# Kernel optimization log

Hardware: AMD Instinct MI355X
Metric: run time of the kernel (lower is better)

The kernel has to match this reference:

```python
import jax, jax.numpy as jnp
import numpy as np

EPS = 1e-5


def _ligru_layer(x, W, U, gamma, beta):
    """One bidirectional LiGRU layer. x: (B,T,F) -> (B,T,2H)."""
    B = x.shape[0]
    H = U.shape[1]
    # bidirectional: stack forward copy and time-flipped copy along batch
    x2 = jnp.concatenate([x, x[:, ::-1]], axis=0)  # (2B, T, F)
    w = jnp.einsum('btf,gf->btg', x2, W)           # (2B, T, 2H)
    # training-mode BatchNorm1d over flattened (2B*T, 2H), biased variance
    flat = w.reshape(-1, w.shape[-1])
    mean = flat.mean(axis=0)
    var = flat.var(axis=0)
    w = (w - mean) * jax.lax.rsqrt(var + EPS) * gamma + beta

    def step(h, wt):
        gates = wt + h @ U.T            # (2B, 2H)
        at, zt = gates[:, :H], gates[:, H:]
        z = jax.nn.sigmoid(zt)
        h = z * h + (1.0 - z) * jax.nn.relu(at)
        return h, h

    h0 = jnp.zeros((w.shape[0], H), dtype=w.dtype)
    _, hs = jax.lax.scan(step, h0, jnp.swapaxes(w, 0, 1))  # (T, 2B, H)
    hs = jnp.swapaxes(hs, 0, 1)                            # (2B, T, H)
    h_f, h_b = hs[:B], hs[B:, ::-1]                        # un-flip backward dir
    return jnp.concatenate([h_f, h_b], axis=2)             # (B, T, 2H)


def setup_inputs() -> dict:
    key = jax.random.key(0)
    ks = jax.random.split(key, 9)
    B, T, F, H = 16, 500, 512, 1024
    return {
        'x': jax.random.normal(ks[0], (B, T, F), jnp.float32),
        'w0': jax.random.normal(ks[1], (2 * H, F), jnp.float32) * (1.0 / np.sqrt(F)),
        'u0': jax.random.normal(ks[2], (2 * H, H), jnp.float32) * (1.0 / np.sqrt(H)),
        'g0': jax.random.uniform(ks[3], (2 * H,), jnp.float32, 0.5, 1.5),
        'b0': jax.random.normal(ks[4], (2 * H,), jnp.float32) * 0.1,
        'w1': jax.random.normal(ks[5], (2 * H, 2 * H), jnp.float32) * (1.0 / np.sqrt(2 * H)),
        'u1': jax.random.normal(ks[6], (2 * H, H), jnp.float32) * (1.0 / np.sqrt(H)),
        'g1': jax.random.uniform(ks[7], (2 * H,), jnp.float32, 0.5, 1.5),
        'b1': jax.random.normal(ks[8], (2 * H,), jnp.float32) * 0.1,
    }


def reference(x, w0, u0, g0, b0, w1, u1, g1, b1):
    h = _ligru_layer(x, w0, u0, g0, b0)   # (B, T, 2H)
    h = _ligru_layer(h, w1, u1, g1, b1)   # (B, T, 2H)
    return h
```

## Files before the change

kernel.cpp:

```cpp
#include <hip/hip_runtime.h>
#include <stdint.h>

#define KT 500
#define KH 1024
#define KG 2048

typedef short bf16x8 __attribute__((ext_vector_type(8)));
typedef float f32x4 __attribute__((ext_vector_type(4)));

__device__ __forceinline__ unsigned short f2bf(float f){
  union { float f; unsigned int i; } u; u.f = f;
  unsigned int x = u.i;
  return (unsigned short)((x + 0x7fffu + ((x >> 16) & 1u)) >> 16);
}
__device__ __forceinline__ float bf2f(unsigned short h){
  union { unsigned int i; float f; } u; u.i = ((unsigned int)h) << 16;
  return u.f;
}

__device__ __forceinline__ void load_b128_dev(uint4& dst, const void* p){
  asm volatile("global_load_dwordx4 %0, %1, off sc1"
               : "=v"(dst) : "v"(p) : "memory");
}
__device__ __forceinline__ void store_b32_dev(void* p, unsigned int v){
  asm volatile("global_store_dword %0, %1, off sc1"
               :: "v"(p), "v"(v) : "memory");
}
__device__ __forceinline__ void wait_vm0(){
  asm volatile("s_waitcnt vmcnt(0)" ::: "memory");
}

__global__ __launch_bounds__(256) void castk(const float* __restrict__ s,
                                             unsigned short* __restrict__ d, int n4){
  int i = blockIdx.x*256 + threadIdx.x;
  if (i >= n4) return;
  float4 v = ((const float4*)s)[i];
  unsigned int lo = (unsigned int)f2bf(v.x) | ((unsigned int)f2bf(v.y) << 16);
  unsigned int hi = (unsigned int)f2bf(v.z) | ((unsigned int)f2bf(v.w) << 16);
  ((uint2*)d)[i] = make_uint2(lo, hi);
}

template<int MODE, int KDIM>
__global__ __launch_bounds__(256) void gemm_bn(
    const unsigned short* __restrict__ A,
    const unsigned short* __restrict__ Bw,
    unsigned short* __restrict__ Wout)
{
  __shared__ __attribute__((aligned(16))) unsigned short As[128*72];
  __shared__ __attribute__((aligned(16))) unsigned short Bs[128*72];
  const int tid = threadIdx.x;
  const int lane = tid & 63, wid = tid >> 6;
  const int ntile = blockIdx.x, mtile = blockIdx.y;
  const int arow_loc = tid >> 3;
  const int k8 = tid & 7;

  long abaseLo[4], abaseHi[4], bbase[4];
  #pragma unroll
  for (int i = 0; i < 4; i++){
    int r = mtile*128 + i*32 + arow_loc;
    int s = r / KT;
    int t = r - s*KT;
    if (MODE == 0){
      abaseLo[i] = (s < 16) ? (long)((s*KT + t)*512)
                            : (long)(((s-16)*KT + (KT-1-t))*512);
      abaseHi[i] = 0;
    } else {
      int sp = s & 15;
      int rev = (s >= 16);
      abaseLo[i] = (long)((sp*KT + (rev ? KT-1-t : t)) * KH);
      abaseHi[i] = (long)(((16+sp)*KT + (rev ? t : KT-1-t)) * KH);
    }
    bbase[i] = (long)(ntile*128 + i*32 + arow_loc) * KDIM;
  }

  f32x4 acc[4][4];
  #pragma unroll
  for (int a=0;a<4;a++)
    #pragma unroll
    for (int b=0;b<4;b++)
      acc[a][b] = (f32x4){0.f,0.f,0.f,0.f};

  const int mhalf = wid & 1, nhalf = wid >> 1;
  const int lrow = lane & 15, quad = lane >> 4;

  for (int k0 = 0; k0 < KDIM; k0 += 64){
    const int kel = k0 + k8*8;
    #pragma unroll
    for (int i = 0; i < 4; i++){
      long aoff;
      if (MODE == 0) aoff = abaseLo[i] + kel;
      else           aoff = (kel < KH) ? (abaseLo[i] + kel) : (abaseHi[i] + (kel - KH));
      uint4 va = *(const uint4*)(A + aoff);
      uint4 vb = *(const uint4*)(Bw + bbase[i] + kel);
      *(uint4*)&As[(i*32 + arow_loc)*72 + k8*8] = va;
      *(uint4*)&Bs[(i*32 + arow_loc)*72 + k8*8] = vb;
    }
    __syncthreads();
    #pragma unroll
    for (int kk = 0; kk < 64; kk += 32){
      bf16x8 af[4], bfr[4];
      #pragma unroll
      for (int mt=0; mt<4; mt++)
        af[mt] = *(const bf16x8*)&As[(mhalf*64 + mt*16 + lrow)*72 + kk + quad*8];
      #pragma unroll
      for (int nt=0; nt<4; nt++)
        bfr[nt] = *(const bf16x8*)&Bs[(nhalf*64 + nt*16 + lrow)*72 + kk + quad*8];
      #pragma unroll
      for (int mt=0; mt<4; mt++)
        #pragma unroll
        for (int nt=0; nt<4; nt++)
          acc[mt][nt] = __builtin_amdgcn_mfma_f32_16x16x32_bf16(af[mt], bfr[nt], acc[mt][nt], 0, 0, 0);
    }
    __syncthreads();
  }

  #pragma unroll
  for (int mt=0; mt<4; mt++)
    #pragma unroll
    for (int nt=0; nt<4; nt++)
      #pragma unroll
      for (int r=0; r<4; r++){
        int grow = mtile*128 + mhalf*64 + mt*16 + quad*4 + r;
        int gcol = ntile*128 + nhalf*64 + nt*16 + lrow;
        Wout[(long)grow*KG + gcol] = f2bf(acc[mt][nt][r]);
      }
}

__global__ __launch_bounds__(256) void bn_partial(const unsigned short* __restrict__ W,
                                                  float* __restrict__ part){
  const int blk = blockIdx.x, tid = threadIdx.x;
  const int c0 = tid*8;
  float s[8], qq[8];
  #pragma unroll
  for (int j=0;j<8;j++){ s[j]=0.f; qq[j]=0.f; }
  const unsigned short* base = W + (long)blk*128*KG + c0;
  for (int r=0;r<128;r++){
    uint4 v = *(const uint4*)(base + (long)r*KG);
    unsigned int w[4] = {v.x, v.y, v.z, v.w};
    #pragma unroll
    for (int p=0;p<4;p++){
      union { unsigned int i; float f; } lo, hi;
      lo.i = w[p] << 16;
      hi.i = w[p] & 0xffff0000u;
      s[2*p]   += lo.f; qq[2*p]   += lo.f*lo.f;
      s[2*p+1] += hi.f; qq[2*p+1] += hi.f*hi.f;
    }
  }
  float* pd = part + (long)blk*4096;
  #pragma unroll
  for (int j=0;j<8;j++){ pd[c0+j] = s[j]; pd[KG + c0 + j] = qq[j]; }
}

__global__ __launch_bounds__(256) void bn_final(const float* __restrict__ part,
                                                const float* __restrict__ gamma,
                                                const float* __restrict__ beta,
                                                float* __restrict__ scsh){
  int g = blockIdx.x*256 + threadIdx.x;
  float s=0.f, qq=0.f;
  for (int b=0;b<125;b++){ s += part[(long)b*4096 + g]; qq += part[(long)b*4096 + KG + g]; }
  float mean = s * (1.f/16000.f);
  float var  = qq * (1.f/16000.f) - mean*mean;
  float sc = gamma[g] * rsqrtf(var + 1e-5f);
  scsh[g]      = sc;
  scsh[KG + g] = beta[g] - mean*sc;
}

template<int LAYER>
__global__ __launch_bounds__(256, 1) void recur(
    const unsigned short* __restrict__ Ub,
    const unsigned short* __restrict__ Wn,
    const float* __restrict__ scsh,
    unsigned short* __restrict__ hbuf,
    int* __restrict__ flags,
    unsigned short* __restrict__ hsOut,
    float* __restrict__ out)
{
  __shared__ __attribute__((aligned(16))) unsigned short Ush[32*1032];
  __shared__ __attribute__((aligned(16))) unsigned short hsh[32*1032];
  __shared__ float gA[32*20];
  __shared__ float gZ[32*20];
  __shared__ float hown[512];
  __shared__ float scA[16], shA[16], scZ[16], shZ[16];

  const int tid = threadIdx.x;
  const int q = blockIdx.x;
  const int ga = q*16;

  #pragma unroll
  for (int i=0;i<16;i++){
    int c = i*256 + tid;
    int row = c >> 7, k8c = c & 127;
    int grow = (row < 16) ? (ga + row) : (KH + ga + row - 16);
    uint4 v = *(const uint4*)(Ub + (long)grow*KH + k8c*8);
    *(uint4*)&Ush[row*1032 + k8c*8] = v;
  }
  if (tid < 64){
    int j = tid & 15, w = tid >> 4;
    if      (w==0) scA[j] = scsh[ga+j];
    else if (w==1) shA[j] = scsh[KG + ga + j];
    else if (w==2) scZ[j] = scsh[KH + ga + j];
    else           shZ[j] = scsh[KG + KH + ga + j];
  }
  hown[tid] = 0.f; hown[tid+256] = 0.f;
  __syncthreads();

  const int lane = tid & 63, wid = tid >> 6;
  const int lrow = lane & 15, quad = lane >> 4;
  const int mhalf = wid & 1, ghalf = wid >> 1;
  const int es = tid >> 3, ep = tid & 7;
  const int r0 = tid >> 7, kc = tid & 127;

  for (int t = 0; t < KT; t++){
    const unsigned short* wr = Wn + (long)(es*KT + t)*KG + ga + 2*ep;
    unsigned int wa01 = *(const unsigned int*)(wr);
    unsigned int wz01 = *(const unsigned int*)(wr + KH);
    asm volatile("" ::: "memory");

    if (t > 0 && tid < 64){
      while (__hip_atomic_load(&flags[(t-1)*64 + tid], __ATOMIC_RELAXED,
                               __HIP_MEMORY_SCOPE_AGENT) == 0){}
    }
    __syncthreads();

    const unsigned short* hb = hbuf + (t & 1)*32768 + r0*KH + kc*8;
    uint4 hreg[16];
    #pragma unroll
    for (int i=0;i<16;i++)
      load_b128_dev(hreg[i], hb + i*2048);
    wait_vm0();
    #pragma unroll
    for (int i=0;i<16;i++)
      *(uint4*)&hsh[(2*i + r0)*1032 + kc*8] = hreg[i];
    __syncthreads();

    f32x4 a0 = (f32x4){0,0,0,0}, a1 = a0, a2 = a0, a3 = a0;
    const unsigned short* ar = &hsh[(mhalf*16 + lrow)*1032 + quad*8];
    const unsigned short* br = &Ush[(ghalf*16 + lrow)*1032 + quad*8];
    #pragma unroll
    for (int k0=0;k0<KH;k0+=128){
      a0 = __builtin_amdgcn_mfma_f32_16x16x32_bf16(*(const bf16x8*)(ar+k0),    *(const bf16x8*)(br+k0),    a0,0,0,0);
      a1 = __builtin_amdgcn_mfma_f32_16x16x32_bf16(*(const bf16x8*)(ar+k0+32), *(const bf16x8*)(br+k0+32), a1,0,0,0);
      a2 = __builtin_amdgcn_mfma_f32_16x16x32_bf16(*(const bf16x8*)(ar+k0+64), *(const bf16x8*)(br+k0+64), a2,0,0,0);
      a3 = __builtin_amdgcn_mfma_f32_16x16x32_bf16(*(const bf16x8*)(ar+k0+96), *(const bf16x8*)(br+k0+96), a3,0,0,0);
    }
    f32x4 accs = (a0 + a1) + (a2 + a3);
    float* gd = ghalf ? gZ : gA;
    #pragma unroll
    for (int r=0;r<4;r++)
      gd[(mhalf*16 + quad*4 + r)*20 + lrow] = accs[r];
    __syncthreads();

    float2 gav = *(const float2*)&gA[es*20 + 2*ep];
    float2 gzv = *(const float2*)&gZ[es*20 + 2*ep];
    float2 hpv = *(const float2*)&hown[es*16 + 2*ep];
    float2 scav = *(const float2*)&scA[2*ep];
    float2 shav = *(const float2*)&shA[2*ep];
    float2 sczv = *(const float2*)&scZ[2*ep];
    float2 shzv = *(const float2*)&shZ[2*ep];
    float aa0 = gav.x + bf2f((unsigned short)(wa01 & 0xffff)) * scav.x + shav.x;
    float aa1 = gav.y + bf2f((unsigned short)(wa01 >> 16))    * scav.y + shav.y;
    float zz0 = gzv.x + bf2f((unsigned short)(wz01 & 0xffff)) * sczv.x + shzv.x;
    float zz1 = gzv.y + bf2f((unsigned short)(wz01 >> 16))    * sczv.y + shzv.y;
    float z0 = 1.f/(1.f + __expf(-zz0));
    float z1 = 1.f/(1.f + __expf(-zz1));
    float hn0 = z0*hpv.x + (1.f - z0)*fmaxf(aa0, 0.f);
    float hn1 = z1*hpv.y + (1.f - z1)*fmaxf(aa1, 0.f);
    *(float2*)&hown[es*16 + 2*ep] = make_float2(hn0, hn1);

    unsigned int hpack = (unsigned int)f2bf(hn0) | ((unsigned int)f2bf(hn1) << 16);
    store_b32_dev(hbuf + ((t+1)&1)*32768 + es*KH + ga + 2*ep, hpack);
    wait_vm0();
    __syncthreads();
    if (tid == 0)
      __hip_atomic_store(&flags[t*64 + q], 1, __ATOMIC_RELAXED, __HIP_MEMORY_SCOPE_AGENT);

    if (LAYER == 0){
      *(unsigned int*)&hsOut[(long)(es*KT + t)*KH + ga + 2*ep] = hpack;
    } else {
      if (es < 16)
        *(float2*)&out[(long)(es*KT + t)*KG + ga + 2*ep] = make_float2(hn0, hn1);
      else
        *(float2*)&out[(long)((es-16)*KT + (KT-1-t))*KG + KH + ga + 2*ep] = make_float2(hn0, hn1);
    }
  }
}

extern "C" void kernel_launch(void* const* d_in, const int* in_sizes, int n_in,
                              void* d_out, int out_size, void* d_ws, size_t ws_size,
                              hipStream_t stream)
{
  const float* x  = (const float*)d_in[0];
  const float* w0 = (const float*)d_in[1];
  const float* u0 = (const float*)d_in[2];
  const float* g0 = (const float*)d_in[3];
  const float* b0 = (const float*)d_in[4];
  const float* w1 = (const float*)d_in[5];
  const float* u1 = (const float*)d_in[6];
  const float* g1 = (const float*)d_in[7];
  const float* b1 = (const float*)d_in[8];
  float* out = (float*)d_out;

  char* p = (char*)d_ws;
  auto alloc = [&](size_t n){ char* r = p; p += (n + 255) & ~(size_t)255; return r; };
  unsigned short* xb   = (unsigned short*)alloc((size_t)16*KT*512*2);
  unsigned short* w0b  = (unsigned short*)alloc((size_t)KG*512*2);
  unsigned short* u0b  = (unsigned short*)alloc((size_t)KG*KH*2);
  unsigned short* w1b  = (unsigned short*)alloc((size_t)KG*KG*2);
  unsigned short* u1b  = (unsigned short*)alloc((size_t)KG*KH*2);
  unsigned short* wbuf = (unsigned short*)alloc((size_t)32*KT*KG*2);
  unsigned short* hs0  = (unsigned short*)alloc((size_t)32*KT*KH*2);
  float* part          = (float*)alloc((size_t)125*4096*4);
  float* scsh          = (float*)alloc((size_t)2*KG*4);
  unsigned short* hbuf = (unsigned short*)alloc((size_t)2*2*32*KH*2);
  int* flags           = (int*)alloc((size_t)2*KT*64*4);

  auto cast = [&](const float* s, unsigned short* d, int n){
    int n4 = n >> 2;
    castk<<<(n4+255)/256, 256, 0, stream>>>(s, d, n4);
  };
  cast(x,  xb,  16*KT*512);
  cast(w0, w0b, KG*512);
  cast(u0, u0b, KG*KH);
  cast(w1, w1b, KG*KG);
  cast(u1, u1b, KG*KH);
  hipMemsetAsync(hbuf,  0, (size_t)2*2*32*KH*2, stream);
  hipMemsetAsync(flags, 0, (size_t)2*KT*64*4,  stream);

  gemm_bn<0,512><<<dim3(16,125), 256, 0, stream>>>(xb, w0b, wbuf);
  bn_partial<<<125,256,0,stream>>>(wbuf, part);
  bn_final<<<8,256,0,stream>>>(part, g0, b0, scsh);
  recur<0><<<64,256,0,stream>>>(u0b, wbuf, scsh, hbuf, flags, hs0, (float*)nullptr);

  gemm_bn<1,2048><<<dim3(16,125), 256, 0, stream>>>(hs0, w1b, wbuf);
  bn_partial<<<125,256,0,stream>>>(wbuf, part);
  bn_final<<<8,256,0,stream>>>(part, g1, b1, scsh);
  recur<1><<<64,256,0,stream>>>(u1b, wbuf, scsh, hbuf + 2*32*KH, flags + KT*64,
                                (unsigned short*)nullptr, out);
}
```

Baseline: 4.577 ms.

## Keep U fragments in registers and load h directly into MFMA operands

The recurrent kernel now holds its slice of U as bf16 MFMA fragments in VGPRs and loads the previous hidden state straight from global memory into A-operand registers. This drops the LDS staging of both h and U and one block-wide barrier per step. The K dimension is split across wave pairs, and the two partial sums are combined through shared memory with an extra barrier. Each wave now polls the flags of the blocks it reads, and the previous h stays in a register. Register pressure rises a lot (32 bf16x8 U fragments plus 16 h loads), which could cause spills.

Measured after the change: 5.225 ms. +14.2%, slower.

```diff
diff --git a/kernel.cpp b/kernel.cpp
--- a/kernel.cpp
+++ b/kernel.cpp
@@ -18,9 +18,10 @@
   return u.f;
 }
 
-__device__ __forceinline__ void load_b128_dev(uint4& dst, const void* p){
-  asm volatile("global_load_dwordx4 %0, %1, off sc1"
-               : "=v"(dst) : "v"(p) : "memory");
+template<int OFF>
+__device__ __forceinline__ void load_b128_dev_off(uint4& dst, const void* p){
+  asm volatile("global_load_dwordx4 %0, %1, off offset:%c2 sc1"
+               : "=v"(dst) : "v"(p), "i"(OFF) : "memory");
 }
 __device__ __forceinline__ void store_b32_dev(void* p, unsigned int v){
   asm volatile("global_store_dword %0, %1, off sc1"
@@ -175,40 +176,37 @@
     unsigned short* __restrict__ hsOut,
     float* __restrict__ out)
 {
-  __shared__ __attribute__((aligned(16))) unsigned short Ush[32*1032];
-  __shared__ __attribute__((aligned(16))) unsigned short hsh[32*1032];
   __shared__ float gA[32*20];
   __shared__ float gZ[32*20];
-  __shared__ float hown[512];
-  __shared__ float scA[16], shA[16], scZ[16], shZ[16];
 
   const int tid = threadIdx.x;
   const int q = blockIdx.x;
   const int ga = q*16;
-
-  #pragma unroll
-  for (int i=0;i<16;i++){
-    int c = i*256 + tid;
-    int row = c >> 7, k8c = c & 127;
-    int grow = (row < 16) ? (ga + row) : (KH + ga + row - 16);
-    uint4 v = *(const uint4*)(Ub + (long)grow*KH + k8c*8);
-    *(uint4*)&Ush[row*1032 + k8c*8] = v;
-  }
-  if (tid < 64){
-    int j = tid & 15, w = tid >> 4;
-    if      (w==0) scA[j] = scsh[ga+j];
-    else if (w==1) shA[j] = scsh[KG + ga + j];
-    else if (w==2) scZ[j] = scsh[KH + ga + j];
-    else           shZ[j] = scsh[KG + KH + ga + j];
-  }
-  hown[tid] = 0.f; hown[tid+256] = 0.f;
-  __syncthreads();
-
   const int lane = tid & 63, wid = tid >> 6;
   const int lrow = lane & 15, quad = lane >> 4;
-  const int mhalf = wid & 1, ghalf = wid >> 1;
+  const int m = wid & 1, kh = wid >> 1;
   const int es = tid >> 3, ep = tid & 7;
-  const int r0 = tid >> 7, kc = tid & 127;
+
+  bf16x8 ufA[16], ufZ[16];
+  {
+    const unsigned short* ua = Ub + (long)(ga + lrow)*KH + kh*512 + quad*8;
+    const unsigned short* uz = ua + (long)KH*KH;
+    #pragma unroll
+    for (int c=0;c<16;c++){
+      ufA[c] = *(const bf16x8*)(ua + c*32);
+      ufZ[c] = *(const bf16x8*)(uz + c*32);
+    }
+  }
+
+  float2 scav = *(const float2*)&scsh[ga + 2*ep];
+  float2 shav = *(const float2*)&scsh[KG + ga + 2*ep];
+  float2 sczv = *(const float2*)&scsh[KH + ga + 2*ep];
+  float2 shzv = *(const float2*)&scsh[KG + KH + ga + 2*ep];
+  float2 hprev = make_float2(0.f, 0.f);
+
+  const long aoff = (long)(m*16 + lrow)*KH + kh*512 + quad*8;
+  const unsigned short* hb0 = hbuf + aoff;
+  const unsigned short* hb1 = hbuf + 32768 + aoff;
 
   for (int t = 0; t < KT; t++){
     const unsigned short* wr = Wn + (long)(es*KT + t)*KG + ga + 2*ep;
@@ -216,56 +214,65 @@
     unsigned int wz01 = *(const unsigned int*)(wr + KH);
     asm volatile("" ::: "memory");
 
-    if (t > 0 && tid < 64){
-      while (__hip_atomic_load(&flags[(t-1)*64 + tid], __ATOMIC_RELAXED,
+    if (t > 0){
+      const int fl = (t-1)*64 + kh*32 + (lane & 31);
+      while (__hip_atomic_load(&flags[fl], __ATOMIC_RELAXED,
                                __HIP_MEMORY_SCOPE_AGENT) == 0){}
     }
-    __syncthreads();
-
-    const unsigned short* hb = hbuf + (t & 1)*32768 + r0*KH + kc*8;
-    uint4 hreg[16];
-    #pragma unroll
-    for (int i=0;i<16;i++)
-      load_b128_dev(hreg[i], hb + i*2048);
+
+    const unsigned short* hb = (t & 1) ? hb1 : hb0;
+    uint4 af[16];
+    #define LDAF(i) load_b128_dev_off<(i)*64>(af[i], hb)
+    LDAF(0);  LDAF(1);  LDAF(2);  LDAF(3);
+    LDAF(4);  LDAF(5);  LDAF(6);  LDAF(7);
+    LDAF(8);  LDAF(9);  LDAF(10); LDAF(11);
+    LDAF(12); LDAF(13); LDAF(14); LDAF(15);
+    #undef LDAF
     wait_vm0();
-    #pragma unroll
-    for (int i=0;i<16;i++)
-      *(uint4*)&hsh[(2*i + r0)*1032 + kc*8] = hreg[i];
-    __syncthreads();
-
-    f32x4 a0 = (f32x4){0,0,0,0}, a1 = a0, a2 = a0, a3 = a0;
-    const unsigned short* ar = &hsh[(mhalf*16 + lrow)*1032 + quad*8];
-    const unsigned short* br = &Ush[(ghalf*16 + lrow)*1032 + quad*8];
-    #pragma unroll
-    for (int k0=0;k0<KH;k0+=128){
-      a0 = __builtin_amdgcn_mfma_f32_16x16x32_bf16(*(const bf16x8*)(ar+k0),    *(const bf16x8*)(br+k0),    a0,0,0,0);
-      a1 = __builtin_amdgcn_mfma_f32_16x16x32_bf16(*(const bf16x8*)(ar+k0+32), *(const bf16x8*)(br+k0+32), a1,0,0,0);
-      a2 = __builtin_amdgcn_mfma_f32_16x16x32_bf16(*(const bf16x8*)(ar+k0+64), *(const bf16x8*)(br+k0+64), a2,0,0,0);
-      a3 = __builtin_amdgcn_mfma_f32_16x16x32_bf16(*(const bf16x8*)(ar+k0+96), *(const bf16x8*)(br+k0+96), a3,0,0,0);
-    }
-    f32x4 accs = (a0 + a1) + (a2 + a3);
-    float* gd = ghalf ? gZ : gA;
-    #pragma unroll
-    for (int r=0;r<4;r++)
-      gd[(mhalf*16 + quad*4 + r)*20 + lrow] = accs[r];
+    __builtin_amdgcn_sched_barrier(0);
+
+    f32x4 aA0 = (f32x4){0,0,0,0}, aA1 = aA0, aZ0 = aA0, aZ1 = aA0;
+    #pragma unroll
+    for (int c=0;c<16;c+=2){
+      bf16x8 x0 = *(bf16x8*)&af[c];
+      bf16x8 x1 = *(bf16x8*)&af[c+1];
+      aA0 = __builtin_amdgcn_mfma_f32_16x16x32_bf16(x0, ufA[c],   aA0, 0,0,0);
+      aZ0 = __builtin_amdgcn_mfma_f32_16x16x32_bf16(x0, ufZ[c],   aZ0, 0,0,0);
+      aA1 = __builtin_amdgcn_mfma_f32_16x16x32_bf16(x1, ufA[c+1], aA1, 0,0,0);
+      aZ1 = __builtin_amdgcn_mfma_f32_16x16x32_bf16(x1, ufZ[c+1], aZ1, 0,0,0);
+    }
+    f32x4 accA = aA0 + aA1;
+    f32x4 accZ = aZ0 + aZ1;
+
+    if (kh){
+      #pragma unroll
+      for (int r=0;r<4;r++){
+        gA[(m*16 + quad*4 + r)*20 + lrow] = accA[r];
+        gZ[(m*16 + quad*4 + r)*20 + lrow] = accZ[r];
+      }
+    }
+    __syncthreads();
+    if (!kh){
+      #pragma unroll
+      for (int r=0;r<4;r++){
+        int ix = (m*16 + quad*4 + r)*20 + lrow;
+        gA[ix] += accA[r];
+        gZ[ix] += accZ[r];
+      }
+    }
     __syncthreads();
 
     float2 gav = *(const float2*)&gA[es*20 + 2*ep];
     float2 gzv = *(const float2*)&gZ[es*20 + 2*ep];
-    float2 hpv = *(const float2*)&hown[es*16 + 2*ep];
-    float2 scav = *(const float2*)&scA[2*ep];
-    float2 shav = *(const float2*)&shA[2*ep];
-    float2 sczv = *(const float2*)&scZ[2*ep];
-    float2 shzv = *(const float2*)&shZ[2*ep];
     float aa0 = gav.x + bf2f((unsigned short)(wa01 & 0xffff)) * scav.x + shav.x;
     float aa1 = gav.y + bf2f((unsigned short)(wa01 >> 16))    * scav.y + shav.y;
     float zz0 = gzv.x + bf2f((unsigned short)(wz01 & 0xffff)) * sczv.x + shzv.x;
     float zz1 = gzv.y + bf2f((unsigned short)(wz01 >> 16))    * sczv.y + shzv.y;
     float z0 = 1.f/(1.f + __expf(-zz0));
     float z1 = 1.f/(1.f + __expf(-zz1));
-    float hn0 = z0*hpv.x + (1.f - z0)*fmaxf(aa0, 0.f);
-    float hn1 = z1*hpv.y + (1.f - z1)*fmaxf(aa1, 0.f);
-    *(float2*)&hown[es*16 + 2*ep] = make_float2(hn0, hn1);
+    float hn0 = z0*hprev.x + (1.f - z0)*fmaxf(aa0, 0.f);
+    float hn1 = z1*hprev.y + (1.f - z1)*fmaxf(aa1, 0.f);
+    hprev = make_float2(hn0, hn1);
 
     unsigned int hpack = (unsigned int)f2bf(hn0) | ((unsigned int)f2bf(hn1) << 16);
     store_b32_dev(hbuf + ((t+1)&1)*32768 + es*KH + ga + 2*ep, hpack);
```
